# Performance work log

Measured on AMD Instinct MI355X. Metric: run time of the kernel, lower is better.

## Reference

```python
import jax, jax.numpy as jnp
import numpy as np

K = 8  # args.k


def setup_inputs() -> dict:
    key = jax.random.key(0)
    k1, k2, k3 = jax.random.split(key, 3)
    b, n_pre, n_cur = 1, 8192, 16384
    pre_xyzs = jax.random.normal(k1, (b, 3, n_pre), dtype=jnp.float32)
    cur_xyzs = jax.random.normal(k2, (b, 3, n_cur), dtype=jnp.float32)
    # UpsampleNumLayer output range: sigmoid * (max_upsample_num - 1) + 1  in [1, 8]
    upsample_num = jax.random.uniform(k3, (b, n_pre), dtype=jnp.float32) * 7.0 + 1.0
    return {"pre_xyzs": pre_xyzs, "cur_xyzs": cur_xyzs, "upsample_num": upsample_num}


def _sqdist(a, b):
    # a: (b, n, 3), b: (b, m, 3) -> (b, n, m) squared euclidean distances
    return ((a * a).sum(-1)[:, :, None]
            + (b * b).sum(-1)[:, None, :]
            - 2.0 * jnp.einsum('bnc,bmc->bnm', a, b))


def reference(pre_xyzs, cur_xyzs, upsample_num):
    # pre_xyzs: (b, 3, n_pre); cur_xyzs: (b, 3, n_cur); upsample_num: (b, n_pre)
    pre_t = pre_xyzs.transpose(0, 2, 1)  # (b, n_pre, 3)
    cur_t = cur_xyzs.transpose(0, 2, 1)  # (b, n_cur, 3)

    # knnquery_heap(1, pre, cur): nearest pre index for each cur point -> (b, n_cur)
    cur2pre = jnp.argmin(_sqdist(cur_t, pre_t), axis=-1)

    # knnquery_heap(K, cur, pre): K nearest cur indices for each pre point -> (b, n_pre, K)
    _, knn_idx = jax.lax.top_k(-_sqdist(pre_t, cur_t), K)

    # real_center: gather cur2pre at knn_idx -> (b, n_pre, K)
    real_center = jax.vmap(lambda c2p, idx: c2p[idx])(cur2pre, knn_idx)
    expect_center = jnp.arange(pre_xyzs.shape[2])[None, :, None]  # (1, n_pre, 1)
    mask = (expect_center == real_center).astype(pre_xyzs.dtype)  # (b, n_pre, K)

    # knn_xyzs: gather cur_xyzs columns at knn_idx -> (b, 3, n_pre, K)
    knn_xyzs = jax.vmap(lambda pts, idx: pts[:, idx])(cur_xyzs, knn_idx)

    diff = knn_xyzs - pre_xyzs[..., None]              # (b, 3, n_pre, K)
    dist = jnp.sqrt((diff * diff).sum(axis=1))         # (b, n_pre, K), L2 over channel dim
    mean_distance = (dist * mask).sum(axis=-1) / upsample_num  # (b, n_pre)
    return mean_distance
```

## Files before the change

### kernel.cpp

```cpp
#include <hip/hip_runtime.h>

#define N_PRE 8192
#define N_CUR 16384
#define KNN   8


#define MAPPED_INF 0xFF800000u

#define NITER  8
#define ATILE  1024
#define BTILE  2048

__device__ __forceinline__ unsigned key_of_bits(unsigned b) {
    return b ^ (0x80000000u | (unsigned)((int)b >> 31));
}
__device__ __forceinline__ float float_of_key(unsigned k) {
    unsigned b = k ^ (0x80000000u | ~(unsigned)((int)k >> 31));
    return __uint_as_float(b);
}

__global__ __launch_bounds__(256) void prep_kernel(
        const float* __restrict__ pre, const float* __restrict__ cur,
        float4* __restrict__ pre4, float4* __restrict__ cur4) {
    int i = blockIdx.x * 256 + threadIdx.x;
    if (i < N_CUR) {
        float x = cur[i], y = cur[N_CUR + i], z = cur[2 * N_CUR + i];
        cur4[i] = make_float4(x, y, z, fmaf(x, x, fmaf(y, y, z * z)));
    }
    if (i < N_PRE) {
        float x = pre[i], y = pre[N_PRE + i], z = pre[2 * N_PRE + i];
        pre4[i] = make_float4(-2.f * x, -2.f * y, -2.f * z,
                              fmaf(x, x, fmaf(y, y, z * z)));
    }
}

__device__ __forceinline__ void pop_top8(float d, float& t8, unsigned& ld,
                                         unsigned& li, int jbase) {
    unsigned long long m = __ballot(d < t8);
    while (m) {
        int src = __ffsll(m) - 1;
        unsigned fdb = (unsigned)__builtin_amdgcn_readlane(__float_as_int(d), src);
        unsigned kd = key_of_bits(fdb);
        unsigned kj = (unsigned)(jbase + src);
        unsigned ud = (unsigned)__builtin_amdgcn_update_dpp(
            0, (int)ld, 0x111, 0xF, 0xF, false);
        unsigned uj = (unsigned)__builtin_amdgcn_update_dpp(
            0, (int)li, 0x111, 0xF, 0xF, false);
        bool hi = kd < ud;
        bool lo = kd < ld;
        ld = hi ? ud : (lo ? kd : ld);
        li = hi ? uj : (lo ? kj : li);
        unsigned k7 = (unsigned)__builtin_amdgcn_readlane((int)ld, 7);
        t8 = float_of_key(k7);
        m = (m & (m - 1)) & __ballot(d < t8);
    }
}

__global__ __launch_bounds__(1024, 8) void fused_ab(
        const float4* __restrict__ pre4, const float4* __restrict__ cur4,
        unsigned* __restrict__ c2p, unsigned* __restrict__ lists) {
    __shared__ float4 sA[ATILE];
    __shared__ float4 sB[BTILE];

    const int tid  = threadIdx.x;
    const int lane = tid & 63;
    const int w    = tid >> 6;
    const bool isB = (w < 8);

    const int ia = blockIdx.x * 16 + w * 2;
    const int wa = w - 8;
    const int j0 = blockIdx.x * 32 + wa * 4;

    float4 p0, p1, c0, c1, c2, c3;
    if (isB) {
        p0 = pre4[ia];
        p1 = pre4[ia + 1];
    } else {
        c0 = cur4[j0 + 0];
        c1 = cur4[j0 + 1];
        c2 = cur4[j0 + 2];
        c3 = cur4[j0 + 3];
    }

    const float INF = __int_as_float(0x7F800000);
    unsigned ld0 = MAPPED_INF, li0 = 0, ld1 = MAPPED_INF, li1 = 0;
    float t80 = INF, t81 = INF;
    float b0 = INF, b1 = INF, b2 = INF, b3 = INF;
    int   i0 = 0,  i1 = 0,  i2 = 0,  i3 = 0;

    for (int it = 0; it < NITER; ++it) {
        __syncthreads();
        sB[tid]        = cur4[it * BTILE + tid];
        sB[tid + 1024] = cur4[it * BTILE + 1024 + tid];
        sA[tid]        = pre4[it * ATILE + tid];
        __syncthreads();

        if (isB) {
#pragma unroll 4
            for (int s = 0; s < BTILE; s += 64) {
                float4 c = sB[s + lane];
                float d0 = fmaf(p0.x, c.x, fmaf(p0.y, c.y, fmaf(p0.z, c.z, c.w)));
                float d1 = fmaf(p1.x, c.x, fmaf(p1.y, c.y, fmaf(p1.z, c.z, c.w)));
                const int jbase = it * BTILE + s;
                pop_top8(d0, t80, ld0, li0, jbase);
                pop_top8(d1, t81, ld1, li1, jbase);
            }
        } else {
#pragma unroll 4
            for (int s = 0; s < ATILE; s += 64) {
                float4 q = sA[s + lane];
                int idx = it * ATILE + s + lane;
                float d; bool c;
                d = fmaf(q.x, c0.x, fmaf(q.y, c0.y, fmaf(q.z, c0.z, q.w)));
                c = d < b0; b0 = c ? d : b0; i0 = c ? idx : i0;
                d = fmaf(q.x, c1.x, fmaf(q.y, c1.y, fmaf(q.z, c1.z, q.w)));
                c = d < b1; b1 = c ? d : b1; i1 = c ? idx : i1;
                d = fmaf(q.x, c2.x, fmaf(q.y, c2.y, fmaf(q.z, c2.z, q.w)));
                c = d < b2; b2 = c ? d : b2; i2 = c ? idx : i2;
                d = fmaf(q.x, c3.x, fmaf(q.y, c3.y, fmaf(q.z, c3.z, q.w)));
                c = d < b3; b3 = c ? d : b3; i3 = c ? idx : i3;
            }
        }
    }

    if (!isB) {
        unsigned long long v0 =
            (((unsigned long long)key_of_bits(__float_as_uint(b0))) << 32) | (unsigned)i0;
        unsigned long long v1 =
            (((unsigned long long)key_of_bits(__float_as_uint(b1))) << 32) | (unsigned)i1;
        unsigned long long v2 =
            (((unsigned long long)key_of_bits(__float_as_uint(b2))) << 32) | (unsigned)i2;
        unsigned long long v3 =
            (((unsigned long long)key_of_bits(__float_as_uint(b3))) << 32) | (unsigned)i3;
#pragma unroll
        for (int off = 32; off > 0; off >>= 1) {
            unsigned long long o;
            o = __shfl_xor(v0, off); v0 = (o < v0) ? o : v0;
            o = __shfl_xor(v1, off); v1 = (o < v1) ? o : v1;
            o = __shfl_xor(v2, off); v2 = (o < v2) ? o : v2;
            o = __shfl_xor(v3, off); v3 = (o < v3) ? o : v3;
        }
        unsigned r = (unsigned)v0;
        r = (lane == 1) ? (unsigned)v1 : r;
        r = (lane == 2) ? (unsigned)v2 : r;
        r = (lane == 3) ? (unsigned)v3 : r;
        if (lane < 4) c2p[j0 + lane] = r;
    } else {
        if (lane < 8) {
            lists[ia * 8 + lane] = li0;
            lists[(ia + 1) * 8 + lane] = li1;
        }
    }
}

__global__ __launch_bounds__(256) void finalize_kernel(
        const float4* __restrict__ pre4, const float4* __restrict__ cur4,
        const float* __restrict__ ups,
        const unsigned* __restrict__ c2p, const unsigned* __restrict__ lists,
        float* __restrict__ out) {
    const int t    = blockIdx.x * 256 + threadIdx.x;
    const int pg   = t >> 3;
    const int slot = t & 7;

    unsigned j = lists[t];
    float4 cc = cur4[j];
    float4 pp = pre4[pg];
    float px = -0.5f * pp.x, py = -0.5f * pp.y, pz = -0.5f * pp.z;
    float dx = cc.x - px, dy = cc.y - py, dz = cc.z - pz;
    float dsq = fmaf(dx, dx, fmaf(dy, dy, dz * dz));
    float acc = (c2p[j] == (unsigned)pg) ? sqrtf(dsq) : 0.f;

    acc += __shfl_xor(acc, 1);
    acc += __shfl_xor(acc, 2);
    acc += __shfl_xor(acc, 4);
    if (slot == 0) out[pg] = acc / ups[pg];
}

extern "C" void kernel_launch(void* const* d_in, const int* in_sizes, int n_in,
                              void* d_out, int out_size, void* d_ws, size_t ws_size,
                              hipStream_t stream) {
    const float* pre = (const float*)d_in[0];
    const float* cur = (const float*)d_in[1];
    const float* ups = (const float*)d_in[2];
    float* out = (float*)d_out;

    char* ws = (char*)d_ws;
    unsigned* c2p   = (unsigned*)ws;
    float4*   pre4  = (float4*)(ws + 65536);
    float4*   cur4  = (float4*)(ws + 65536 + 131072);
    unsigned* lists = (unsigned*)(ws + 65536 + 131072 + 262144);

    prep_kernel<<<N_CUR / 256, 256, 0, stream>>>(pre, cur, pre4, cur4);

    fused_ab<<<512, 1024, 0, stream>>>(pre4, cur4, c2p, lists);

    finalize_kernel<<<N_PRE * 8 / 256, 256, 0, stream>>>(
        pre4, cur4, ups, c2p, lists, out);
}
```

Baseline: 118.8 us.

## Split fused kernel into heterogeneous 512-thread blocks by role

Replaces the 1024-thread blocks, whose waves split between a KNN top-8 role and a nearest-center role under shared barriers, with separate 512-thread blocks. Even block indices do only the top-8 search over cur points and odd indices do only the argmin over pre points, each with its own shared tile. This removes the lockstep coupling where the fast argmin waves waited at barriers for the slower ballot-driven top-8 waves, and lets each block type run at its own pace. In exchange each role stages its own tiles, so global-to-shared loads are no longer shared between the two roles.

```diff
diff --git a/kernel.cpp b/kernel.cpp
--- a/kernel.cpp
+++ b/kernel.cpp
@@ -7,9 +7,7 @@
 
 #define MAPPED_INF 0xFF800000u
 
-#define NITER  8
-#define ATILE  1024
-#define BTILE  2048
+#define TILE 2048
 
 __device__ __forceinline__ unsigned key_of_bits(unsigned b) {
     return b ^ (0x80000000u | (unsigned)((int)b >> 31));
@@ -56,60 +54,68 @@
     }
 }
 
-__global__ __launch_bounds__(1024, 8) void fused_ab(
+__global__ __launch_bounds__(512, 8) void fused_het(
         const float4* __restrict__ pre4, const float4* __restrict__ cur4,
         unsigned* __restrict__ c2p, unsigned* __restrict__ lists) {
-    __shared__ float4 sA[ATILE];
-    __shared__ float4 sB[BTILE];
+    __shared__ float4 sbuf[TILE];
 
     const int tid  = threadIdx.x;
     const int lane = tid & 63;
     const int w    = tid >> 6;
-    const bool isB = (w < 8);
+    const int bid  = blockIdx.x >> 1;
 
-    const int ia = blockIdx.x * 16 + w * 2;
-    const int wa = w - 8;
-    const int j0 = blockIdx.x * 32 + wa * 4;
+    if ((blockIdx.x & 1) == 0) {
+        const int ia = bid * 16 + w * 2;
+        const int ib = ia + 1;
 
-    float4 p0, p1, c0, c1, c2, c3;
-    if (isB) {
-        p0 = pre4[ia];
-        p1 = pre4[ia + 1];
-    } else {
-        c0 = cur4[j0 + 0];
-        c1 = cur4[j0 + 1];
-        c2 = cur4[j0 + 2];
-        c3 = cur4[j0 + 3];
-    }
+        const float4 p0 = pre4[ia];
+        const float4 p1 = pre4[ib];
 
-    const float INF = __int_as_float(0x7F800000);
-    unsigned ld0 = MAPPED_INF, li0 = 0, ld1 = MAPPED_INF, li1 = 0;
-    float t80 = INF, t81 = INF;
-    float b0 = INF, b1 = INF, b2 = INF, b3 = INF;
-    int   i0 = 0,  i1 = 0,  i2 = 0,  i3 = 0;
+        const float INF = __int_as_float(0x7F800000);
+        unsigned ld0 = MAPPED_INF, li0 = 0, ld1 = MAPPED_INF, li1 = 0;
+        float t80 = INF, t81 = INF;
 
-    for (int it = 0; it < NITER; ++it) {
-        __syncthreads();
-        sB[tid]        = cur4[it * BTILE + tid];
-        sB[tid + 1024] = cur4[it * BTILE + 1024 + tid];
-        sA[tid]        = pre4[it * ATILE + tid];
-        __syncthreads();
+        for (int tile = 0; tile < N_CUR; tile += TILE) {
+            __syncthreads();
+            for (int k = tid; k < TILE; k += 512) sbuf[k] = cur4[tile + k];
+            __syncthreads();
 
-        if (isB) {
 #pragma unroll 4
-            for (int s = 0; s < BTILE; s += 64) {
-                float4 c = sB[s + lane];
+            for (int s = 0; s < TILE; s += 64) {
+                float4 c = sbuf[s + lane];
                 float d0 = fmaf(p0.x, c.x, fmaf(p0.y, c.y, fmaf(p0.z, c.z, c.w)));
                 float d1 = fmaf(p1.x, c.x, fmaf(p1.y, c.y, fmaf(p1.z, c.z, c.w)));
-                const int jbase = it * BTILE + s;
+                const int jbase = tile + s;
                 pop_top8(d0, t80, ld0, li0, jbase);
                 pop_top8(d1, t81, ld1, li1, jbase);
             }
-        } else {
+        }
+
+        if (lane < 8) {
+            lists[ia * 8 + lane] = li0;
+            lists[ib * 8 + lane] = li1;
+        }
+    } else {
+        const int j0 = bid * 32 + w * 4;
+
+        const float4 c0 = cur4[j0 + 0];
+        const float4 c1 = cur4[j0 + 1];
+        const float4 c2 = cur4[j0 + 2];
+        const float4 c3 = cur4[j0 + 3];
+
+        const float INF = __int_as_float(0x7F800000);
+        float b0 = INF, b1 = INF, b2 = INF, b3 = INF;
+        int   i0 = 0,  i1 = 0,  i2 = 0,  i3 = 0;
+
+        for (int tile = 0; tile < N_PRE; tile += TILE) {
+            __syncthreads();
+            for (int k = tid; k < TILE; k += 512) sbuf[k] = pre4[tile + k];
+            __syncthreads();
+
 #pragma unroll 4
-            for (int s = 0; s < ATILE; s += 64) {
-                float4 q = sA[s + lane];
-                int idx = it * ATILE + s + lane;
+            for (int s = 0; s < TILE; s += 64) {
+                float4 q = sbuf[s + lane];
+                int idx = tile + s + lane;
                 float d; bool c;
                 d = fmaf(q.x, c0.x, fmaf(q.y, c0.y, fmaf(q.z, c0.z, q.w)));
                 c = d < b0; b0 = c ? d : b0; i0 = c ? idx : i0;
@@ -121,9 +127,7 @@
                 c = d < b3; b3 = c ? d : b3; i3 = c ? idx : i3;
             }
         }
-    }
 
-    if (!isB) {
         unsigned long long v0 =
             (((unsigned long long)key_of_bits(__float_as_uint(b0))) << 32) | (unsigned)i0;
         unsigned long long v1 =
@@ -145,11 +149,6 @@
         r = (lane == 2) ? (unsigned)v2 : r;
         r = (lane == 3) ? (unsigned)v3 : r;
         if (lane < 4) c2p[j0 + lane] = r;
-    } else {
-        if (lane < 8) {
-            lists[ia * 8 + lane] = li0;
-            lists[(ia + 1) * 8 + lane] = li1;
-        }
     }
 }
 
@@ -192,7 +191,7 @@
 
     prep_kernel<<<N_CUR / 256, 256, 0, stream>>>(pre, cur, pre4, cur4);
 
-    fused_ab<<<512, 1024, 0, stream>>>(pre4, cur4, c2p, lists);
+    fused_het<<<1024, 512, 0, stream>>>(pre4, cur4, c2p, lists);
 
     finalize_kernel<<<N_PRE * 8 / 256, 256, 0, stream>>>(
         pre4, cur4, ups, c2p, lists, out);
```

Result: slower. 130.4 us (+9.7%).

## Fold prep kernel into fused KNN kernel and halve block size

Applied to the files above, without the earlier changes.

Removes the separate prep kernel that packed coordinates into float4 with squared norms. The packing now happens while each tile is staged into shared memory, and the finalize kernel reads the raw planar inputs. Blocks shrink from 1024 to 512 threads over twice as many blocks, with smaller tiles and more iterations. This saves one launch and the workspace round-trip. In exchange, the packing arithmetic is repeated in every block, strided planar loads replace float4 loads, and synchronisation barriers double.

```diff
diff --git a/kernel.cpp b/kernel.cpp
--- a/kernel.cpp
+++ b/kernel.cpp
@@ -7,9 +7,9 @@
 
 #define MAPPED_INF 0xFF800000u
 
-#define NITER  8
-#define ATILE  1024
-#define BTILE  2048
+#define NITER  16
+#define BTILE  1024
+#define ATILE  512
 
 __device__ __forceinline__ unsigned key_of_bits(unsigned b) {
     return b ^ (0x80000000u | (unsigned)((int)b >> 31));
@@ -17,21 +17,6 @@
 __device__ __forceinline__ float float_of_key(unsigned k) {
     unsigned b = k ^ (0x80000000u | ~(unsigned)((int)k >> 31));
     return __uint_as_float(b);
-}
-
-__global__ __launch_bounds__(256) void prep_kernel(
-        const float* __restrict__ pre, const float* __restrict__ cur,
-        float4* __restrict__ pre4, float4* __restrict__ cur4) {
-    int i = blockIdx.x * 256 + threadIdx.x;
-    if (i < N_CUR) {
-        float x = cur[i], y = cur[N_CUR + i], z = cur[2 * N_CUR + i];
-        cur4[i] = make_float4(x, y, z, fmaf(x, x, fmaf(y, y, z * z)));
-    }
-    if (i < N_PRE) {
-        float x = pre[i], y = pre[N_PRE + i], z = pre[2 * N_PRE + i];
-        pre4[i] = make_float4(-2.f * x, -2.f * y, -2.f * z,
-                              fmaf(x, x, fmaf(y, y, z * z)));
-    }
 }
 
 __device__ __forceinline__ void pop_top8(float d, float& t8, unsigned& ld,
@@ -56,30 +41,42 @@
     }
 }
 
-__global__ __launch_bounds__(1024, 8) void fused_ab(
-        const float4* __restrict__ pre4, const float4* __restrict__ cur4,
+__device__ __forceinline__ float4 pack_pre_q(const float* __restrict__ pre,
+                                             int i) {
+    float x = pre[i], y = pre[N_PRE + i], z = pre[2 * N_PRE + i];
+    return make_float4(-2.f * x, -2.f * y, -2.f * z,
+                       fmaf(x, x, fmaf(y, y, z * z)));
+}
+__device__ __forceinline__ float4 pack_cur_q(const float* __restrict__ cur,
+                                             int j) {
+    float x = cur[j], y = cur[N_CUR + j], z = cur[2 * N_CUR + j];
+    return make_float4(x, y, z, fmaf(x, x, fmaf(y, y, z * z)));
+}
+
+__global__ __launch_bounds__(512, 8) void fused_ab(
+        const float* __restrict__ pre, const float* __restrict__ cur,
         unsigned* __restrict__ c2p, unsigned* __restrict__ lists) {
+    __shared__ float4 sB[BTILE];
     __shared__ float4 sA[ATILE];
-    __shared__ float4 sB[BTILE];
 
     const int tid  = threadIdx.x;
     const int lane = tid & 63;
     const int w    = tid >> 6;
-    const bool isB = (w < 8);
-
-    const int ia = blockIdx.x * 16 + w * 2;
-    const int wa = w - 8;
-    const int j0 = blockIdx.x * 32 + wa * 4;
+    const bool isB = (w < 4);
+
+    const int ia = blockIdx.x * 8 + w * 2;
+    const int wa = w - 4;
+    const int j0 = blockIdx.x * 16 + wa * 4;
 
     float4 p0, p1, c0, c1, c2, c3;
     if (isB) {
-        p0 = pre4[ia];
-        p1 = pre4[ia + 1];
+        p0 = pack_pre_q(pre, ia);
+        p1 = pack_pre_q(pre, ia + 1);
     } else {
-        c0 = cur4[j0 + 0];
-        c1 = cur4[j0 + 1];
-        c2 = cur4[j0 + 2];
-        c3 = cur4[j0 + 3];
+        c0 = pack_cur_q(cur, j0 + 0);
+        c1 = pack_cur_q(cur, j0 + 1);
+        c2 = pack_cur_q(cur, j0 + 2);
+        c3 = pack_cur_q(cur, j0 + 3);
     }
 
     const float INF = __int_as_float(0x7F800000);
@@ -90,9 +87,20 @@
 
     for (int it = 0; it < NITER; ++it) {
         __syncthreads();
-        sB[tid]        = cur4[it * BTILE + tid];
-        sB[tid + 1024] = cur4[it * BTILE + 1024 + tid];
-        sA[tid]        = pre4[it * ATILE + tid];
+        {
+            int e0 = it * BTILE + tid;
+            int e1 = e0 + 512;
+            float x0 = cur[e0], y0 = cur[N_CUR + e0], z0 = cur[2 * N_CUR + e0];
+            float x1 = cur[e1], y1 = cur[N_CUR + e1], z1 = cur[2 * N_CUR + e1];
+            int e2 = it * ATILE + tid;
+            float px = pre[e2], py = pre[N_PRE + e2], pz = pre[2 * N_PRE + e2];
+            sB[tid]       = make_float4(x0, y0, z0,
+                                        fmaf(x0, x0, fmaf(y0, y0, z0 * z0)));
+            sB[tid + 512] = make_float4(x1, y1, z1,
+                                        fmaf(x1, x1, fmaf(y1, y1, z1 * z1)));
+            sA[tid]       = make_float4(-2.f * px, -2.f * py, -2.f * pz,
+                                        fmaf(px, px, fmaf(py, py, pz * pz)));
+        }
         __syncthreads();
 
         if (isB) {
@@ -154,7 +162,7 @@
 }
 
 __global__ __launch_bounds__(256) void finalize_kernel(
-        const float4* __restrict__ pre4, const float4* __restrict__ cur4,
+        const float* __restrict__ pre, const float* __restrict__ cur,
         const float* __restrict__ ups,
         const unsigned* __restrict__ c2p, const unsigned* __restrict__ lists,
         float* __restrict__ out) {
@@ -163,10 +171,9 @@
     const int slot = t & 7;
 
     unsigned j = lists[t];
-    float4 cc = cur4[j];
-    float4 pp = pre4[pg];
-    float px = -0.5f * pp.x, py = -0.5f * pp.y, pz = -0.5f * pp.z;
-    float dx = cc.x - px, dy = cc.y - py, dz = cc.z - pz;
+    float cx = cur[j], cy = cur[N_CUR + j], cz = cur[2 * N_CUR + j];
+    float px = pre[pg], py = pre[N_PRE + pg], pz = pre[2 * N_PRE + pg];
+    float dx = cx - px, dy = cy - py, dz = cz - pz;
     float dsq = fmaf(dx, dx, fmaf(dy, dy, dz * dz));
     float acc = (c2p[j] == (unsigned)pg) ? sqrtf(dsq) : 0.f;
 
@@ -186,14 +193,10 @@
 
     char* ws = (char*)d_ws;
     unsigned* c2p   = (unsigned*)ws;
-    float4*   pre4  = (float4*)(ws + 65536);
-    float4*   cur4  = (float4*)(ws + 65536 + 131072);
-    unsigned* lists = (unsigned*)(ws + 65536 + 131072 + 262144);
-
-    prep_kernel<<<N_CUR / 256, 256, 0, stream>>>(pre, cur, pre4, cur4);
-
-    fused_ab<<<512, 1024, 0, stream>>>(pre4, cur4, c2p, lists);
+    unsigned* lists = (unsigned*)(ws + 65536);
+
+    fused_ab<<<1024, 512, 0, stream>>>(pre, cur, c2p, lists);
 
     finalize_kernel<<<N_PRE * 8 / 256, 256, 0, stream>>>(
-        pre4, cur4, ups, c2p, lists, out);
-}
+        pre, cur, ups, c2p, lists, out);
+}
```

Measured after the change: 126.5 us. 1.06x slower.
